# Kernel tuning notes

Hardware: AMD Instinct MI355X
Metric: run time of the kernel (lower is better)

The kernel has to match this reference:

```python
import jax, jax.numpy as jnp
import numpy as np

N_USER = 100000
N_ITEM = 50000
N_NODES = N_USER + N_ITEM
N_EDGES = 2000000
N_LAYERS = 3
EMB = 64
BATCH = 2048


def setup_inputs() -> dict:
    key = jax.random.key(0)
    ks = jax.random.split(key, 7)
    return {
        "user_emb": 0.1 * jax.random.normal(ks[0], (N_USER, EMB), dtype=jnp.float32),
        "item_emb": 0.1 * jax.random.normal(ks[1], (N_ITEM, EMB), dtype=jnp.float32),
        "adj_vals": jax.random.uniform(ks[2], (N_EDGES,), dtype=jnp.float32),
        "adj_rows": jax.random.randint(ks[3], (N_EDGES,), 0, N_NODES, dtype=jnp.int32),
        "adj_cols": jax.random.randint(ks[4], (N_EDGES,), 0, N_NODES, dtype=jnp.int32),
        "users": jax.random.randint(ks[5], (BATCH,), 0, N_USER, dtype=jnp.int32),
        "items": jax.random.randint(ks[6], (BATCH,), 0, N_ITEM, dtype=jnp.int32),
    }


def _computer(user_emb, item_emb, adj_vals, adj_rows, adj_cols):
    # LightGCN propagation: emb_{l+1} = A_hat @ emb_l, output = mean over layers 0..L
    all_emb = jnp.concatenate([user_emb, item_emb], axis=0)  # [N, d]
    emb = all_emb
    acc = all_emb
    for _ in range(N_LAYERS):
        msg = adj_vals[:, None] * emb[adj_cols]              # [E, d]
        emb = jax.ops.segment_sum(msg, adj_rows, num_segments=N_NODES)
        acc = acc + emb
    light_out = acc / jnp.float32(N_LAYERS + 1)              # mean over L+1 embeddings
    return light_out[:N_USER], light_out[N_USER:]


def reference(user_emb, item_emb, adj_vals, adj_rows, adj_cols, users, items):
    all_users, all_items = _computer(user_emb, item_emb, adj_vals, adj_rows, adj_cols)
    u = all_users[users]   # [Bu, d]
    i = all_items[items]   # [Bi, d]
    return jax.nn.sigmoid(u @ i.T)  # [Bu, Bi]
```

## Files before the change

### kernel.cpp

```cpp
#include <hip/hip_runtime.h>
#include <hip/hip_bf16.h>


#define EMB 64
#define BSZ 512
#define NBMAX 512
#define BP 1024

__device__ __forceinline__ float bf2f_lo(unsigned int u) {
    return __int_as_float((int)(u << 16));
}
__device__ __forceinline__ float bf2f_hi(unsigned int u) {
    return __int_as_float((int)(u & 0xFFFF0000u));
}
__device__ __forceinline__ float bf2f(unsigned short u) {
    return __int_as_float(((int)u) << 16);
}
__device__ __forceinline__ unsigned short f2bf(float f) {
    union { float f; unsigned int i; } v;
    v.f = f;
    unsigned int lsb = (v.i >> 16) & 1;
    v.i += 0x7fffu + lsb;
    return (unsigned short)(v.i >> 16);
}
__device__ __forceinline__ unsigned int pack2(float a, float b) {
    return (unsigned int)f2bf(a) | ((unsigned int)f2bf(b) << 16);
}

__device__ __forceinline__ int wave_iscan(int v) {
    int lane = threadIdx.x & 63;
#pragma unroll
    for (int off = 1; off < 64; off <<= 1) {
        int x = __shfl_up(v, off, 64);
        if (lane >= off) v += x;
    }
    return v;
}

__global__ void ALGN_init_emb(const float4* __restrict__ ue, const float4* __restrict__ ie,
                              uint4* __restrict__ emb, int* __restrict__ flags,
                              int nFlags, int nUser4, int n4) {
    int t = blockIdx.x * blockDim.x + threadIdx.x;
    if (t < nFlags) flags[t] = 0;
    if (t >= n4) return;
    float4 v = (t < nUser4) ? ue[t] : ie[t - nUser4];
    uint4 o;
    o.x = pack2(v.x, v.y);
    o.y = pack2(v.z, v.w);
    (void)o;
}

__global__ void ALGN_init_emb8(const float4* __restrict__ ue, const float4* __restrict__ ie,
                               uint4* __restrict__ emb, int* __restrict__ flags,
                               int nFlags, int nUser8, int n8) {
    int t = blockIdx.x * blockDim.x + threadIdx.x;
    if (t < nFlags) flags[t] = 0;
    if (t >= n8) return;
    float4 a, b;
    if (t < nUser8) { a = ue[2 * t]; b = ue[2 * t + 1]; }
    else           { a = ie[2 * (t - nUser8)]; b = ie[2 * (t - nUser8) + 1]; }
    uint4 o;
    o.x = pack2(a.x, a.y);
    o.y = pack2(a.z, a.w);
    o.z = pack2(b.x, b.y);
    o.w = pack2(b.z, b.w);
    emb[t] = o;
}

__global__ void ALGN_p1(const int* __restrict__ rows, int* __restrict__ blockHist,
                        int nE, int seg, int nBuckets) {
    __shared__ int h[NBMAX];
    int blk = blockIdx.x;
    for (int i = threadIdx.x; i < nBuckets; i += blockDim.x) h[i] = 0;
    __syncthreads();
    int beg = blk * seg, end = min(beg + seg, nE);
    for (int e = beg + threadIdx.x; e < end; e += blockDim.x)
        atomicAdd(&h[rows[e] >> 9], 1);
    __syncthreads();
    for (int u = threadIdx.x; u < nBuckets; u += blockDim.x)
        blockHist[u * BP + blk] = h[u];
}

__global__ void ALGN_scanA(int* __restrict__ blockHist, int* __restrict__ bucketTotal) {
    __shared__ int wsum[16];
    int b = blockIdx.x, t = threadIdx.x;
    int wid = t >> 6;
    int v = blockHist[b * BP + t];
    int isc = wave_iscan(v);
    if ((t & 63) == 63) wsum[wid] = isc;
    __syncthreads();
    if (t < 64) {
        int s = (t < 16) ? wsum[t] : 0;
        s = wave_iscan(s);
        if (t < 16) wsum[t] = s;
    }
    __syncthreads();
    int incl = isc + ((wid > 0) ? wsum[wid - 1] : 0);
    blockHist[b * BP + t] = incl - v;
    if (t == BP - 1) bucketTotal[b] = incl;
}

__global__ void ALGN_scanB(const int* __restrict__ bucketTotal, int* __restrict__ bucketBase,
                           int nBuckets) {
    __shared__ int wsum[8];
    int t = threadIdx.x;
    int wid = t >> 6;
    int v = (t < nBuckets) ? bucketTotal[t] : 0;
    int isc = wave_iscan(v);
    if ((t & 63) == 63) wsum[wid] = isc;
    __syncthreads();
    if (t < 64) {
        int s = (t < 8) ? wsum[t] : 0;
        s = wave_iscan(s);
        if (t < 8) wsum[t] = s;
    }
    __syncthreads();
    int incl = isc + ((wid > 0) ? wsum[wid - 1] : 0);
    if (t < nBuckets) bucketBase[t] = incl - v;
    if (t == nBuckets - 1) bucketBase[nBuckets] = incl;
}

__global__ void ALGN_p2(const int* __restrict__ rows, const int* __restrict__ cols,
                        const float* __restrict__ vals,
                        const int* __restrict__ blockHist, const int* __restrict__ bucketBase,
                        int2* __restrict__ part, int nE, int seg, int nBuckets) {
    __shared__ int cur[NBMAX];
    int blk = blockIdx.x;
    for (int u = threadIdx.x; u < nBuckets; u += blockDim.x)
        cur[u] = bucketBase[u] + blockHist[u * BP + blk];
    __syncthreads();
    int beg = blk * seg, end = min(beg + seg, nE);
    for (int e = beg + threadIdx.x; e < end; e += blockDim.x) {
        int r = rows[e];
        int u = r >> 9;
        int pos = atomicAdd(&cur[u], 1);
        int lr = r & 511;
        part[pos] = make_int2((lr << 18) | cols[e], __float_as_int(vals[e]));
    }
}

__global__ void ALGN_bsort(const int2* __restrict__ part, const int* __restrict__ bucketBase,
                           int2* __restrict__ pairs, int* __restrict__ rowPtr,
                           int nNodes, int nBuckets, int nE) {
    __shared__ int st[BSZ];
    __shared__ int wsum[8];
    int b = blockIdx.x, t = threadIdx.x;
    int base = bucketBase[b], lim = bucketBase[b + 1];
    if (t < BSZ) st[t] = 0;
    __syncthreads();
    for (int j = base + t; j < lim; j += blockDim.x)
        atomicAdd(&st[part[j].x >> 18], 1);
    __syncthreads();
    int wid = t >> 6;
    int v = (t < BSZ) ? st[t] : 0;
    int isc = wave_iscan(v);
    if ((t & 63) == 63 && wid < 8) wsum[wid] = isc;
    __syncthreads();
    if (t < 64) {
        int s = (t < 8) ? wsum[t] : 0;
        s = wave_iscan(s);
        if (t < 8) wsum[t] = s;
    }
    __syncthreads();
    int excl = isc - v + ((wid > 0 && wid < 8) ? wsum[wid - 1] : 0);
    __syncthreads();
    if (t < BSZ) st[t] = excl;
    int row = b * BSZ + t;
    if (t < BSZ && row < nNodes) rowPtr[row] = base + excl;
    if (b == nBuckets - 1 && t == 0) rowPtr[nNodes] = nE;
    __syncthreads();
    for (int j = base + t; j < lim; j += blockDim.x) {
        int2 p = part[j];
        int lr = p.x >> 18;
        int pos = base + atomicAdd(&st[lr], 1);
        pairs[pos] = make_int2(p.x & 0x3FFFF, p.y);
    }
}

__global__ void ALGN_mark2(const int* __restrict__ rowPtr, const int2* __restrict__ pairs,
                           const int* __restrict__ users, const int* __restrict__ items,
                           int* __restrict__ flag2, int* __restrict__ flagB,
                           int batch, int nUser) {
    int tid = blockIdx.x * blockDim.x + threadIdx.x;
    int idx = tid >> 4;
    int ln  = tid & 15;
    if (idx >= 2 * batch) return;
    int row = (idx < batch) ? users[idx] : (nUser + items[idx - batch]);
    if (ln == 0) { flagB[row] = 1; flag2[row] = 1; }
    int beg = rowPtr[row], end = rowPtr[row + 1];
    for (int j = beg + ln; j < end; j += 16) flag2[pairs[j].x] = 1;
}

__device__ __forceinline__ void acc8(float& s0, float& s1, float& s2, float& s3,
                                     float& s4, float& s5, float& s6, float& s7,
                                     float v, uint4 x) {
    s0 += v * bf2f_lo(x.x); s1 += v * bf2f_hi(x.x);
    s2 += v * bf2f_lo(x.y); s3 += v * bf2f_hi(x.y);
    s4 += v * bf2f_lo(x.z); s5 += v * bf2f_hi(x.z);
    s6 += v * bf2f_lo(x.w); s7 += v * bf2f_hi(x.w);
}

__device__ __forceinline__ void spmm_row(const uint4* __restrict__ cur,
                                         uint4* __restrict__ next,
                                         const int* __restrict__ rowPtr,
                                         const int2* __restrict__ pairs,
                                         int row, int fl) {
    int beg = rowPtr[row];
    int end = rowPtr[row + 1];
    float s0 = 0.f, s1 = 0.f, s2 = 0.f, s3 = 0.f;
    float s4 = 0.f, s5 = 0.f, s6 = 0.f, s7 = 0.f;
    int j = beg;
    for (; j + 4 <= end; j += 4) {
        int2 e0 = pairs[j + 0];
        int2 e1 = pairs[j + 1];
        int2 e2 = pairs[j + 2];
        int2 e3 = pairs[j + 3];
        uint4 x0 = cur[(size_t)e0.x * 8 + fl];
        uint4 x1 = cur[(size_t)e1.x * 8 + fl];
        uint4 x2 = cur[(size_t)e2.x * 8 + fl];
        uint4 x3 = cur[(size_t)e3.x * 8 + fl];
        acc8(s0, s1, s2, s3, s4, s5, s6, s7, __int_as_float(e0.y), x0);
        acc8(s0, s1, s2, s3, s4, s5, s6, s7, __int_as_float(e1.y), x1);
        acc8(s0, s1, s2, s3, s4, s5, s6, s7, __int_as_float(e2.y), x2);
        acc8(s0, s1, s2, s3, s4, s5, s6, s7, __int_as_float(e3.y), x3);
    }
    for (; j < end; ++j) {
        int2 e = pairs[j];
        uint4 x = cur[(size_t)e.x * 8 + fl];
        acc8(s0, s1, s2, s3, s4, s5, s6, s7, __int_as_float(e.y), x);
    }
    uint4 o;
    o.x = pack2(s0, s1);
    o.y = pack2(s2, s3);
    o.z = pack2(s4, s5);
    o.w = pack2(s6, s7);
    next[(size_t)row * 8 + fl] = o;
}

__global__ void ALGN_spmm_csr(const uint4* __restrict__ cur, uint4* __restrict__ next,
                              const int* __restrict__ rowPtr, const int2* __restrict__ pairs,
                              int nNodes) {
    int tid = blockIdx.x * blockDim.x + threadIdx.x;
    int row = tid >> 3;
    int fl  = tid & 7;
    if (row >= nNodes) return;
    spmm_row(cur, next, rowPtr, pairs, row, fl);
}

__global__ void ALGN_spmm_flag(const uint4* __restrict__ cur, uint4* __restrict__ next,
                               const int* __restrict__ rowPtr, const int2* __restrict__ pairs,
                               const int* __restrict__ flag, int nNodes) {
    int tid = blockIdx.x * blockDim.x + threadIdx.x;
    int row = tid >> 3;
    int fl  = tid & 7;
    if (row >= nNodes) return;
    if (!flag[row]) return;
    spmm_row(cur, next, rowPtr, pairs, row, fl);
}

__global__ void ALGN_gather_set(const unsigned short* __restrict__ emb,
                                const int* __restrict__ users, const int* __restrict__ items,
                                float* __restrict__ U, float* __restrict__ I,
                                int batch, int nUser) {
    int t = blockIdx.x * blockDim.x + threadIdx.x;
    if (t >= batch * EMB) return;
    int b = t >> 6, c = t & 63;
    U[t] = bf2f(emb[users[b] * EMB + c]) * 0.25f;
    I[t] = bf2f(emb[(nUser + items[b]) * EMB + c]) * 0.25f;
}

__global__ void ALGN_gather_add(const unsigned short* __restrict__ emb,
                                const int* __restrict__ users, const int* __restrict__ items,
                                float* __restrict__ U, float* __restrict__ I,
                                int batch, int nUser) {
    int t = blockIdx.x * blockDim.x + threadIdx.x;
    if (t >= batch * EMB) return;
    int b = t >> 6, c = t & 63;
    U[t] += bf2f(emb[users[b] * EMB + c]) * 0.25f;
    I[t] += bf2f(emb[(nUser + items[b]) * EMB + c]) * 0.25f;
}

__global__ void ALGN_gemm_sigmoid(const float* __restrict__ U, const float* __restrict__ I,
                                  float* __restrict__ out, int B) {
    __shared__ float su[32][EMB + 1];
    __shared__ float si[32][EMB + 1];
    int tx = threadIdx.x, ty = threadIdx.y;
    int row0 = blockIdx.y * 32, col0 = blockIdx.x * 32;
    int tid = ty * 16 + tx;
    for (int k = tid; k < 32 * EMB; k += 256) {
        int r = k >> 6, c = k & 63;
        su[r][c] = U[(row0 + r) * EMB + c];
        si[r][c] = I[(col0 + r) * EMB + c];
    }
    __syncthreads();
    float s00 = 0.f, s01 = 0.f, s10 = 0.f, s11 = 0.f;
#pragma unroll
    for (int k = 0; k < EMB; ++k) {
        float a0 = su[2 * ty][k],     a1 = su[2 * ty + 1][k];
        float b0 = si[2 * tx][k],     b1 = si[2 * tx + 1][k];
        s00 += a0 * b0; s01 += a0 * b1;
        s10 += a1 * b0; s11 += a1 * b1;
    }
    int r0 = row0 + 2 * ty, c0 = col0 + 2 * tx;
    out[(size_t)r0 * B + c0]           = 1.f / (1.f + __expf(-s00));
    out[(size_t)r0 * B + c0 + 1]       = 1.f / (1.f + __expf(-s01));
    out[(size_t)(r0 + 1) * B + c0]     = 1.f / (1.f + __expf(-s10));
    out[(size_t)(r0 + 1) * B + c0 + 1] = 1.f / (1.f + __expf(-s11));
}

extern "C" void kernel_launch(void* const* d_in, const int* in_sizes, int n_in,
                              void* d_out, int out_size, void* d_ws, size_t ws_size,
                              hipStream_t stream) {
    const float* user_emb = (const float*)d_in[0];
    const float* item_emb = (const float*)d_in[1];
    const float* adj_vals = (const float*)d_in[2];
    const int*   adj_rows = (const int*)d_in[3];
    const int*   adj_cols = (const int*)d_in[4];
    const int*   users    = (const int*)d_in[5];
    const int*   items    = (const int*)d_in[6];
    float* out = (float*)d_out;

    const int nUserF = in_sizes[0];
    const int nItemF = in_sizes[1];
    const int nEdges = in_sizes[2];
    const int batch  = in_sizes[5];
    const int nUser  = nUserF / EMB;
    const int totalF = nUserF + nItemF;
    const int nNodes = totalF / EMB;
    const int n8     = totalF / 8;
    const int nBuckets = (nNodes + BSZ - 1) / BSZ;
    const int seg    = (nEdges + BP - 1) / BP;

    unsigned short* embA = (unsigned short*)d_ws;
    unsigned short* embB = embA + totalF;
    float* Ub = (float*)(embB + totalF);
    float* Ib = Ub + (size_t)batch * EMB;
    int2*  pairs = (int2*)(Ib + (size_t)batch * EMB);
    int2*  part  = pairs + nEdges;
    int*   rowPtr = (int*)(part + nEdges);
    int*   blockHist   = rowPtr + (nNodes + 1);
    int*   bucketTotal = blockHist + NBMAX * BP;
    int*   bucketBase  = bucketTotal + NBMAX;
    int*   flag2 = bucketBase + (NBMAX + 1);
    int*   flagB = flag2 + nNodes;

    ALGN_init_emb8<<<(n8 + 255) / 256, 256, 0, stream>>>(
        (const float4*)user_emb, (const float4*)item_emb, (uint4*)embA,
        flag2, 2 * nNodes, nUserF / 8, n8);

    ALGN_p1<<<BP, 256, 0, stream>>>(adj_rows, blockHist, nEdges, seg, nBuckets);
    ALGN_scanA<<<nBuckets, BP, 0, stream>>>(blockHist, bucketTotal);
    ALGN_scanB<<<1, 512, 0, stream>>>(bucketTotal, bucketBase, nBuckets);
    ALGN_p2<<<BP, 256, 0, stream>>>(adj_rows, adj_cols, adj_vals,
                                    blockHist, bucketBase, part, nEdges, seg, nBuckets);
    ALGN_bsort<<<nBuckets, 1024, 0, stream>>>(part, bucketBase, pairs, rowPtr,
                                              nNodes, nBuckets, nEdges);

    ALGN_mark2<<<(2 * batch * 16 + 255) / 256, 256, 0, stream>>>(
        rowPtr, pairs, users, items, flag2, flagB, batch, nUser);

    ALGN_gather_set<<<(batch * EMB + 255) / 256, 256, 0, stream>>>(
        embA, users, items, Ub, Ib, batch, nUser);

    const int fullBlocks = (nNodes * 8 + 255) / 256;

    ALGN_spmm_csr<<<fullBlocks, 256, 0, stream>>>(
        (const uint4*)embA, (uint4*)embB, rowPtr, pairs, nNodes);
    ALGN_gather_add<<<(batch * EMB + 255) / 256, 256, 0, stream>>>(
        embB, users, items, Ub, Ib, batch, nUser);

    ALGN_spmm_flag<<<fullBlocks, 256, 0, stream>>>(
        (const uint4*)embB, (uint4*)embA, rowPtr, pairs, flag2, nNodes);
    ALGN_gather_add<<<(batch * EMB + 255) / 256, 256, 0, stream>>>(
        embA, users, items, Ub, Ib, batch, nUser);

    ALGN_spmm_flag<<<fullBlocks, 256, 0, stream>>>(
        (const uint4*)embA, (uint4*)embB, rowPtr, pairs, flagB, nNodes);
    ALGN_gather_add<<<(batch * EMB + 255) / 256, 256, 0, stream>>>(
        embB, users, items, Ub, Ib, batch, nUser);

    dim3 gg(batch / 32, batch / 32);
    dim3 gb(16, 16);
    ALGN_gemm_sigmoid<<<gg, gb, 0, stream>>>(Ub, Ib, out, batch);
}
```

Measured before the change: 285.3 us.

## Merge init with histogram and mark with gather, double partition block count

Merges embedding init and the row-histogram pass into one launch with block-range dispatch, and merges the mark and first-gather kernels the same way, which removes two kernel launches. It also doubles the partition block count BP to 2048, so scanA now scans two histogram entries per thread and p2 runs with more, smaller segments. The extra blocks enlarge the blockHist array; that is safe only if the workspace and the unseen p2/bsort code still hold with the larger BP.

```diff
diff --git a/kernel.cpp b/kernel.cpp
--- a/kernel.cpp
+++ b/kernel.cpp
@@ -5,7 +5,7 @@
 #define EMB 64
 #define BSZ 512
 #define NBMAX 512
-#define BP 1024
+#define BP 2048
 
 __device__ __forceinline__ float bf2f_lo(unsigned int u) {
     return __int_as_float((int)(u << 16));
@@ -37,67 +37,59 @@
     return v;
 }
 
-__global__ void ALGN_init_emb(const float4* __restrict__ ue, const float4* __restrict__ ie,
-                              uint4* __restrict__ emb, int* __restrict__ flags,
-                              int nFlags, int nUser4, int n4) {
-    int t = blockIdx.x * blockDim.x + threadIdx.x;
-    if (t < nFlags) flags[t] = 0;
-    if (t >= n4) return;
-    float4 v = (t < nUser4) ? ue[t] : ie[t - nUser4];
-    uint4 o;
-    o.x = pack2(v.x, v.y);
-    o.y = pack2(v.z, v.w);
-    (void)o;
-}
-
-__global__ void ALGN_init_emb8(const float4* __restrict__ ue, const float4* __restrict__ ie,
-                               uint4* __restrict__ emb, int* __restrict__ flags,
-                               int nFlags, int nUser8, int n8) {
-    int t = blockIdx.x * blockDim.x + threadIdx.x;
-    if (t < nFlags) flags[t] = 0;
-    if (t >= n8) return;
-    float4 a, b;
-    if (t < nUser8) { a = ue[2 * t]; b = ue[2 * t + 1]; }
-    else           { a = ie[2 * (t - nUser8)]; b = ie[2 * (t - nUser8) + 1]; }
-    uint4 o;
-    o.x = pack2(a.x, a.y);
-    o.y = pack2(a.z, a.w);
-    o.z = pack2(b.x, b.y);
-    o.w = pack2(b.z, b.w);
-    emb[t] = o;
-}
-
-__global__ void ALGN_p1(const int* __restrict__ rows, int* __restrict__ blockHist,
-                        int nE, int seg, int nBuckets) {
+__global__ void ALGN_init_p1(const float4* __restrict__ ue, const float4* __restrict__ ie,
+                             uint4* __restrict__ emb, int* __restrict__ flags, int nFlags,
+                             int nUser8, int n8, int initBlocks,
+                             const int* __restrict__ rows, int* __restrict__ blockHist,
+                             int nE, int seg, int nBuckets) {
     __shared__ int h[NBMAX];
-    int blk = blockIdx.x;
-    for (int i = threadIdx.x; i < nBuckets; i += blockDim.x) h[i] = 0;
-    __syncthreads();
-    int beg = blk * seg, end = min(beg + seg, nE);
-    for (int e = beg + threadIdx.x; e < end; e += blockDim.x)
-        atomicAdd(&h[rows[e] >> 9], 1);
-    __syncthreads();
-    for (int u = threadIdx.x; u < nBuckets; u += blockDim.x)
-        blockHist[u * BP + blk] = h[u];
+    if (blockIdx.x < initBlocks) {
+        int t = blockIdx.x * blockDim.x + threadIdx.x;
+        if (t < nFlags) flags[t] = 0;
+        if (t >= n8) return;
+        float4 a, b;
+        if (t < nUser8) { a = ue[2 * t]; b = ue[2 * t + 1]; }
+        else           { a = ie[2 * (t - nUser8)]; b = ie[2 * (t - nUser8) + 1]; }
+        uint4 o;
+        o.x = pack2(a.x, a.y);
+        o.y = pack2(a.z, a.w);
+        o.z = pack2(b.x, b.y);
+        o.w = pack2(b.z, b.w);
+        emb[t] = o;
+    } else {
+        int blk = blockIdx.x - initBlocks;
+        for (int i = threadIdx.x; i < nBuckets; i += blockDim.x) h[i] = 0;
+        __syncthreads();
+        int beg = blk * seg, end = min(beg + seg, nE);
+        for (int e = beg + threadIdx.x; e < end; e += blockDim.x)
+            atomicAdd(&h[rows[e] >> 9], 1);
+        __syncthreads();
+        for (int u = threadIdx.x; u < nBuckets; u += blockDim.x)
+            blockHist[u * BP + blk] = h[u];
+    }
 }
 
 __global__ void ALGN_scanA(int* __restrict__ blockHist, int* __restrict__ bucketTotal) {
     __shared__ int wsum[16];
     int b = blockIdx.x, t = threadIdx.x;
     int wid = t >> 6;
-    int v = blockHist[b * BP + t];
-    int isc = wave_iscan(v);
+    int v0 = blockHist[b * BP + 2 * t];
+    int v1 = blockHist[b * BP + 2 * t + 1];
+    int s = v0 + v1;
+    int isc = wave_iscan(s);
     if ((t & 63) == 63) wsum[wid] = isc;
     __syncthreads();
     if (t < 64) {
-        int s = (t < 16) ? wsum[t] : 0;
-        s = wave_iscan(s);
-        if (t < 16) wsum[t] = s;
+        int x = (t < 16) ? wsum[t] : 0;
+        x = wave_iscan(x);
+        if (t < 16) wsum[t] = x;
     }
     __syncthreads();
     int incl = isc + ((wid > 0) ? wsum[wid - 1] : 0);
-    blockHist[b * BP + t] = incl - v;
-    if (t == BP - 1) bucketTotal[b] = incl;
+    int excl = incl - s;
+    blockHist[b * BP + 2 * t]     = excl;
+    blockHist[b * BP + 2 * t + 1] = excl + v0;
+    if (t == 1023) bucketTotal[b] = incl;
 }
 
 __global__ void ALGN_scanB(const int* __restrict__ bucketTotal, int* __restrict__ bucketBase,
@@ -177,18 +169,28 @@
     }
 }
 
-__global__ void ALGN_mark2(const int* __restrict__ rowPtr, const int2* __restrict__ pairs,
-                           const int* __restrict__ users, const int* __restrict__ items,
-                           int* __restrict__ flag2, int* __restrict__ flagB,
-                           int batch, int nUser) {
-    int tid = blockIdx.x * blockDim.x + threadIdx.x;
-    int idx = tid >> 4;
-    int ln  = tid & 15;
-    if (idx >= 2 * batch) return;
-    int row = (idx < batch) ? users[idx] : (nUser + items[idx - batch]);
-    if (ln == 0) { flagB[row] = 1; flag2[row] = 1; }
-    int beg = rowPtr[row], end = rowPtr[row + 1];
-    for (int j = beg + ln; j < end; j += 16) flag2[pairs[j].x] = 1;
+__global__ void ALGN_mark_gather(const int* __restrict__ rowPtr, const int2* __restrict__ pairs,
+                                 const int* __restrict__ users, const int* __restrict__ items,
+                                 int* __restrict__ flag2, int* __restrict__ flagB,
+                                 int batch, int nUser, int markBlocks,
+                                 const unsigned short* __restrict__ emb,
+                                 float* __restrict__ U, float* __restrict__ I) {
+    if (blockIdx.x < markBlocks) {
+        int tid = blockIdx.x * blockDim.x + threadIdx.x;
+        int idx = tid >> 4;
+        int ln  = tid & 15;
+        if (idx >= 2 * batch) return;
+        int row = (idx < batch) ? users[idx] : (nUser + items[idx - batch]);
+        if (ln == 0) { flagB[row] = 1; flag2[row] = 1; }
+        int beg = rowPtr[row], end = rowPtr[row + 1];
+        for (int j = beg + ln; j < end; j += 16) flag2[pairs[j].x] = 1;
+    } else {
+        int t = (blockIdx.x - markBlocks) * blockDim.x + threadIdx.x;
+        if (t >= batch * EMB) return;
+        int b = t >> 6, c = t & 63;
+        U[t] = bf2f(emb[users[b] * EMB + c]) * 0.25f;
+        I[t] = bf2f(emb[(nUser + items[b]) * EMB + c]) * 0.25f;
+    }
 }
 
 __device__ __forceinline__ void acc8(float& s0, float& s1, float& s2, float& s3,
@@ -258,17 +260,6 @@
     spmm_row(cur, next, rowPtr, pairs, row, fl);
 }
 
-__global__ void ALGN_gather_set(const unsigned short* __restrict__ emb,
-                                const int* __restrict__ users, const int* __restrict__ items,
-                                float* __restrict__ U, float* __restrict__ I,
-                                int batch, int nUser) {
-    int t = blockIdx.x * blockDim.x + threadIdx.x;
-    if (t >= batch * EMB) return;
-    int b = t >> 6, c = t & 63;
-    U[t] = bf2f(emb[users[b] * EMB + c]) * 0.25f;
-    I[t] = bf2f(emb[(nUser + items[b]) * EMB + c]) * 0.25f;
-}
-
 __global__ void ALGN_gather_add(const unsigned short* __restrict__ emb,
                                 const int* __restrict__ users, const int* __restrict__ items,
                                 float* __restrict__ U, float* __restrict__ I,
@@ -344,23 +335,24 @@
     int*   flag2 = bucketBase + (NBMAX + 1);
     int*   flagB = flag2 + nNodes;
 
-    ALGN_init_emb8<<<(n8 + 255) / 256, 256, 0, stream>>>(
+    const int initBlocks = (n8 + 255) / 256;
+    ALGN_init_p1<<<initBlocks + BP, 256, 0, stream>>>(
         (const float4*)user_emb, (const float4*)item_emb, (uint4*)embA,
-        flag2, 2 * nNodes, nUserF / 8, n8);
-
-    ALGN_p1<<<BP, 256, 0, stream>>>(adj_rows, blockHist, nEdges, seg, nBuckets);
-    ALGN_scanA<<<nBuckets, BP, 0, stream>>>(blockHist, bucketTotal);
+        flag2, 2 * nNodes, nUserF / 8, n8, initBlocks,
+        adj_rows, blockHist, nEdges, seg, nBuckets);
+
+    ALGN_scanA<<<nBuckets, 1024, 0, stream>>>(blockHist, bucketTotal);
     ALGN_scanB<<<1, 512, 0, stream>>>(bucketTotal, bucketBase, nBuckets);
     ALGN_p2<<<BP, 256, 0, stream>>>(adj_rows, adj_cols, adj_vals,
                                     blockHist, bucketBase, part, nEdges, seg, nBuckets);
     ALGN_bsort<<<nBuckets, 1024, 0, stream>>>(part, bucketBase, pairs, rowPtr,
                                               nNodes, nBuckets, nEdges);
 
-    ALGN_mark2<<<(2 * batch * 16 + 255) / 256, 256, 0, stream>>>(
-        rowPtr, pairs, users, items, flag2, flagB, batch, nUser);
-
-    ALGN_gather_set<<<(batch * EMB + 255) / 256, 256, 0, stream>>>(
-        embA, users, items, Ub, Ib, batch, nUser);
+    const int markBlocks = (2 * batch * 16 + 255) / 256;
+    const int gsBlocks   = (batch * EMB + 255) / 256;
+    ALGN_mark_gather<<<markBlocks + gsBlocks, 256, 0, stream>>>(
+        rowPtr, pairs, users, items, flag2, flagB, batch, nUser, markBlocks,
+        embA, Ub, Ib);
 
     const int fullBlocks = (nNodes * 8 + 255) / 256;
 
```

New measurement: 280.2 us. No clear change (-1.8%).
